# Kernel tuning notes

Hardware: AMD Instinct MI355X
Metric: run time of the kernel (lower is better)

The kernel has to match this reference:

```python
import jax, jax.numpy as jnp
import numpy as np

BN_EPS = 1e-5


def setup_inputs() -> dict:
    key = jax.random.key(0)
    ks = jax.random.split(key, 6)
    B, C, K, N = 4, 64, 16, 16384  # batch, feat channels, neighbors, points
    W_OUT = 16  # weightnet output channels (fixed by Linear(16*mlp[-1], ...))
    xyz = jax.random.normal(ks[0], (B, N, 3), dtype=jnp.float32)
    points = jax.random.normal(ks[1], (B, C, K, N), dtype=jnp.float32)
    coordinate = jax.random.normal(ks[2], (B, 3, K, N), dtype=jnp.float32)
    w1 = jax.random.normal(ks[3], (W_OUT, 3), dtype=jnp.float32) * 0.5
    b1 = jnp.zeros((W_OUT,), dtype=jnp.float32)
    lin_w = jax.random.normal(ks[4], (C, W_OUT * C), dtype=jnp.float32) * (1.0 / np.sqrt(W_OUT * C))
    lin_b = jnp.zeros((C,), dtype=jnp.float32)
    gamma = jnp.ones((C,), dtype=jnp.float32)
    beta = jnp.zeros((C,), dtype=jnp.float32)
    return {"xyz": xyz, "points": points, "coordinate": coordinate,
            "w1": w1, "b1": b1, "lin_w": lin_w, "lin_b": lin_b,
            "gamma": gamma, "beta": beta}


def reference(xyz, points, coordinate, w1, b1, lin_w, lin_b, gamma, beta):
    B, C, K, N = points.shape
    # weightnet: 1x1 conv (3 -> 16) + ReLU over coordinate [B,3,K,N] -> [B,16,K,N]
    weights = jax.nn.relu(jnp.einsum('oc,bckn->bokn', w1, coordinate) + b1[None, :, None, None])
    # per-point aggregation: [B,N,C,K] @ [B,N,K,16] -> [B,N,C,16]
    new_points = jnp.einsum('bckn,bokn->bnco', points, weights)
    new_points = new_points.reshape(B, N, C * 16)  # [B, N, 16*C]
    # linear projection 16*C -> C
    new_points = jnp.einsum('bnk,ok->bno', new_points, lin_w) + lin_b  # [B, N, C]
    # BatchNorm1d over channel dim (training-mode batch stats), layout [B, C, N]
    new_points = new_points.transpose(0, 2, 1)  # [B, C, N]
    mean = jnp.mean(new_points, axis=(0, 2), keepdims=True)
    var = jnp.var(new_points, axis=(0, 2), keepdims=True)
    new_points = (new_points - mean) * jax.lax.rsqrt(var + BN_EPS)
    new_points = new_points * gamma[None, :, None] + beta[None, :, None]
    new_points = jax.nn.relu(new_points)  # [B, C, N]
    return (xyz, new_points)
```

## Files before the change

kernel.cpp:

```cpp
#include <hip/hip_runtime.h>

#define BB 4
#define CC 64
#define KK 16
#define NN 16384
#define NT 64
#define CH 8
#define KS 128

typedef __attribute__((ext_vector_type(8))) short short8;
typedef __attribute__((ext_vector_type(4))) float floatx4;

__device__ __forceinline__ unsigned short f2bf(float x) {
    unsigned u = __builtin_bit_cast(unsigned, x);
    u += 0x7FFFu + ((u >> 16) & 1u);
    return (unsigned short)(u >> 16);
}
__device__ __forceinline__ float bflo(unsigned u) {
    return __builtin_bit_cast(float, u << 16);
}
__device__ __forceinline__ float bfhi(unsigned u) {
    return __builtin_bit_cast(float, u & 0xFFFF0000u);
}

__global__ __launch_bounds__(256, 2)
void fused_main(const float* __restrict__ points,
                const float* __restrict__ coordinate,
                const float* __restrict__ w1,
                const float* __restrict__ b1,
                const float* __restrict__ lin_w,
                float* __restrict__ y_out)
{
    __shared__ __align__(16) unsigned short s_p[CH][NT][24];
    __shared__ __align__(16) unsigned short s_a[NT][KS + 8];
    __shared__ __align__(16) unsigned short s_w[CC][KS + 8];

    const int t    = threadIdx.x;
    const int lane = t & 63;
    const int q    = __builtin_amdgcn_readfirstlane(t >> 6);
    const int r    = lane & 15;
    const int s    = lane >> 4;

    const int bid = blockIdx.x;
    const int b   = bid >> 8;
    const int n0  = (bid & 255) * NT;

    float wreg[4][KK];
    {
        const float* coordB = coordinate + (size_t)b * 3 * KK * NN + n0 + lane;
        float c0[KK], c1[KK], c2[KK];
        #pragma unroll
        for (int k = 0; k < KK; ++k) {
            c0[k] = coordB[(0 * KK + k) * NN];
            c1[k] = coordB[(1 * KK + k) * NN];
            c2[k] = coordB[(2 * KK + k) * NN];
        }
        #pragma unroll
        for (int j = 0; j < 4; ++j) {
            const int o = 4 * q + j;
            const float w1x = w1[o * 3 + 0];
            const float w1y = w1[o * 3 + 1];
            const float w1z = w1[o * 3 + 2];
            const float bo  = b1[o];
            #pragma unroll
            for (int k = 0; k < KK; ++k) {
                float v = fmaf(w1x, c0[k], fmaf(w1y, c1[k], fmaf(w1z, c2[k], bo)));
                wreg[j][k] = fmaxf(v, 0.0f);
            }
        }
    }

    floatx4 acc[4];
    #pragma unroll
    for (int nt = 0; nt < 4; ++nt) acc[nt] = (floatx4){0.f, 0.f, 0.f, 0.f};

    const float* pB = points + (size_t)b * CC * KK * NN + n0;

    for (int c8 = 0; c8 < CC; c8 += CH) {
        __syncthreads();

        #pragma unroll
        for (int w = 0; w < 8; ++w) {
            const int idx = w * 256 + t;
            const int c_l = idx >> 8;
            const int k   = (idx >> 4) & 15;
            const int n4  = (idx & 15) * 4;
            const float4 v =
                *(const float4*)(pB + ((size_t)(c8 + c_l) * KK + k) * NN + n4);
            s_p[c_l][n4 + 0][k] = f2bf(v.x);
            s_p[c_l][n4 + 1][k] = f2bf(v.y);
            s_p[c_l][n4 + 2][k] = f2bf(v.z);
            s_p[c_l][n4 + 3][k] = f2bf(v.w);
        }
        #pragma unroll
        for (int w = 0; w < 8; ++w) {
            const int idx = w * 256 + t;
            const int oc  = idx >> 5;
            const int k4  = (idx & 31) * 4;
            const float4 v =
                *(const float4*)(lin_w + (size_t)oc * 1024 + c8 * 16 + k4);
            ushort4 pk;
            pk.x = f2bf(v.x); pk.y = f2bf(v.y); pk.z = f2bf(v.z); pk.w = f2bf(v.w);
            *(ushort4*)&s_w[oc][k4] = pk;
        }
        __syncthreads();

        #pragma unroll
        for (int c_l = 0; c_l < CH; ++c_l) {
            const uint4 u0 = *(const uint4*)&s_p[c_l][lane][0];
            const uint4 u1 = *(const uint4*)&s_p[c_l][lane][8];
            float p16[16];
            p16[0]  = bflo(u0.x); p16[1]  = bfhi(u0.x);
            p16[2]  = bflo(u0.y); p16[3]  = bfhi(u0.y);
            p16[4]  = bflo(u0.z); p16[5]  = bfhi(u0.z);
            p16[6]  = bflo(u0.w); p16[7]  = bfhi(u0.w);
            p16[8]  = bflo(u1.x); p16[9]  = bfhi(u1.x);
            p16[10] = bflo(u1.y); p16[11] = bfhi(u1.y);
            p16[12] = bflo(u1.z); p16[13] = bfhi(u1.z);
            p16[14] = bflo(u1.w); p16[15] = bfhi(u1.w);
            float a4[4];
            #pragma unroll
            for (int j = 0; j < 4; ++j) {
                float a = 0.f;
                #pragma unroll
                for (int k = 0; k < KK; ++k) a = fmaf(p16[k], wreg[j][k], a);
                a4[j] = a;
            }
            ushort4 pk;
            pk.x = f2bf(a4[0]); pk.y = f2bf(a4[1]);
            pk.z = f2bf(a4[2]); pk.w = f2bf(a4[3]);
            *(ushort4*)&s_a[lane][c_l * 16 + 4 * q] = pk;
        }
        __syncthreads();

        #pragma unroll
        for (int kk = 0; kk < 4; ++kk) {
            const short8 af = *(const short8*)&s_a[16 * q + r][kk * 32 + s * 8];
            #pragma unroll
            for (int nt = 0; nt < 4; ++nt) {
                const short8 bf = *(const short8*)&s_w[nt * 16 + r][kk * 32 + s * 8];
                acc[nt] = __builtin_amdgcn_mfma_f32_16x16x32_bf16(af, bf, acc[nt], 0, 0, 0);
            }
        }
    }

    float* yB = y_out + (size_t)b * CC * NN + n0;
    #pragma unroll
    for (int nt = 0; nt < 4; ++nt) {
        const int oc = nt * 16 + r;
        const float4 v = make_float4(acc[nt][0], acc[nt][1], acc[nt][2], acc[nt][3]);
        *(float4*)(yB + (size_t)oc * NN + 16 * q + 4 * s) = v;
    }
}

__global__ __launch_bounds__(256)
void bn_reduce(const float* __restrict__ y, const float* __restrict__ gamma,
               const float* __restrict__ beta, float* __restrict__ ab)
{
    const int ch = blockIdx.x;
    const int t  = threadIdx.x;
    float s = 0.f, ss = 0.f;
    for (int b = 0; b < BB; ++b) {
        const float4* p = (const float4*)(y + ((size_t)b * CC + ch) * NN);
        for (int i = t; i < NN / 4; i += 256) {
            const float4 v = p[i];
            s  += v.x + v.y + v.z + v.w;
            ss += v.x * v.x + v.y * v.y + v.z * v.z + v.w * v.w;
        }
    }
    #pragma unroll
    for (int m = 1; m < 64; m <<= 1) {
        s  += __shfl_xor(s, m);
        ss += __shfl_xor(ss, m);
    }
    __shared__ float rs[4], rss[4];
    if ((t & 63) == 0) { rs[t >> 6] = s; rss[t >> 6] = ss; }
    __syncthreads();
    if (t == 0) {
        const float S  = rs[0] + rs[1] + rs[2] + rs[3];
        const float SS = rss[0] + rss[1] + rss[2] + rss[3];
        const float inv  = 1.0f / (float)(BB * NN);
        const float mean = S * inv;
        const float var  = SS * inv - mean * mean;
        const float a    = gamma[ch] * rsqrtf(var + 1e-5f);
        ab[ch]      = a;
        ab[CC + ch] = beta[ch] - mean * a;
    }
}

__global__ __launch_bounds__(256)
void bn_apply(float* __restrict__ y, const float* __restrict__ ab)
{
    const size_t i = (size_t)blockIdx.x * 256 + threadIdx.x;
    float4* p = (float4*)y;
    float4 v = p[i];
    const int ch = (int)((i * 4) >> 14) & 63;
    const float a = ab[ch], bb = ab[CC + ch];
    v.x = fmaxf(fmaf(a, v.x, bb), 0.0f);
    v.y = fmaxf(fmaf(a, v.y, bb), 0.0f);
    v.z = fmaxf(fmaf(a, v.z, bb), 0.0f);
    v.w = fmaxf(fmaf(a, v.w, bb), 0.0f);
    p[i] = v;
}

extern "C" void kernel_launch(void* const* d_in, const int* in_sizes, int n_in,
                              void* d_out, int out_size, void* d_ws, size_t ws_size,
                              hipStream_t stream)
{
    const float* xyz        = (const float*)d_in[0];
    const float* points     = (const float*)d_in[1];
    const float* coordinate = (const float*)d_in[2];
    const float* w1         = (const float*)d_in[3];
    const float* b1         = (const float*)d_in[4];
    const float* lin_w      = (const float*)d_in[5];
    const float* gamma      = (const float*)d_in[7];
    const float* beta       = (const float*)d_in[8];

    float* out = (float*)d_out;
    float* ws  = (float*)d_ws;

    const size_t xyz_elems = (size_t)BB * NN * 3;

    hipMemcpyAsync(out, xyz, xyz_elems * sizeof(float),
                   hipMemcpyDeviceToDevice, stream);

    float* y_out = out + xyz_elems;

    fused_main<<<BB * (NN / NT), 256, 0, stream>>>(
        points, coordinate, w1, b1, lin_w, y_out);
    bn_reduce<<<CC, 256, 0, stream>>>(y_out, gamma, beta, ws);
    bn_apply<<<(BB * CC * NN) / 4 / 256, 256, 0, stream>>>(y_out, ws);
}
```

Measured before the change: 488.5 us.

## Load points directly to registers, prepack lin_w fragments, split BN reduce

```diff
diff --git a/kernel.cpp b/kernel.cpp
--- a/kernel.cpp
+++ b/kernel.cpp
@@ -6,46 +6,77 @@
 #define NN 16384
 #define NT 64
 #define CH 8
-#define KS 128
+#define NCH 8
 
 typedef __attribute__((ext_vector_type(8))) short short8;
 typedef __attribute__((ext_vector_type(4))) float floatx4;
-
-__device__ __forceinline__ unsigned short f2bf(float x) {
+typedef __attribute__((ext_vector_type(2))) _Float16 half2v;
+
+__device__ __forceinline__ unsigned short f2bf_rtne(float x) {
     unsigned u = __builtin_bit_cast(unsigned, x);
     u += 0x7FFFu + ((u >> 16) & 1u);
     return (unsigned short)(u >> 16);
 }
-__device__ __forceinline__ float bflo(unsigned u) {
-    return __builtin_bit_cast(float, u << 16);
-}
-__device__ __forceinline__ float bfhi(unsigned u) {
-    return __builtin_bit_cast(float, u & 0xFFFF0000u);
-}
-
-__global__ __launch_bounds__(256, 2)
+
+__device__ __forceinline__ unsigned pack_bf16x2(float lo, float hi) {
+    unsigned a = __builtin_bit_cast(unsigned, lo) + 0x8000u;
+    unsigned b = __builtin_bit_cast(unsigned, hi) + 0x8000u;
+    return __builtin_amdgcn_perm(b, a, 0x07060302u);
+}
+
+__device__ __forceinline__ half2v cvt2h(float a, float b) {
+    return __builtin_bit_cast(half2v, __builtin_amdgcn_cvt_pkrtz(a, b));
+}
+
+#if __has_builtin(__builtin_amdgcn_fdot2)
+#define DOT2(a, b, c) __builtin_amdgcn_fdot2((a), (b), (c), false)
+#else
+__device__ __forceinline__ float dot2_fb(half2v a, half2v b, float c) {
+    return fmaf((float)a[0], (float)b[0], fmaf((float)a[1], (float)b[1], c));
+}
+#define DOT2(a, b, c) dot2_fb((a), (b), (c))
+#endif
+
+__global__ __launch_bounds__(256)
+void prep_bfrag(const float* __restrict__ lin_w, unsigned short* __restrict__ bfrag)
+{
+    const int tid  = blockIdx.x * 256 + threadIdx.x;
+    const int lane = tid & 63;
+    const int g    = tid >> 6;
+    const int ci   = g >> 4;
+    const int kk   = (g >> 2) & 3;
+    const int nt   = g & 3;
+    const int r    = lane & 15;
+    const int sq   = lane >> 4;
+
+    const float* src = lin_w + (size_t)(nt * 16 + r) * 1024 + ci * 128 + kk * 32 + sq * 8;
+    unsigned short v[8];
+    #pragma unroll
+    for (int j = 0; j < 8; ++j) v[j] = f2bf_rtne(src[j]);
+    *(uint4*)(bfrag + ((size_t)g * 64 + lane) * 8) = *(const uint4*)v;
+}
+
+__global__ __launch_bounds__(256, 4)
 void fused_main(const float* __restrict__ points,
                 const float* __restrict__ coordinate,
                 const float* __restrict__ w1,
                 const float* __restrict__ b1,
-                const float* __restrict__ lin_w,
+                const unsigned short* __restrict__ bfrag,
                 float* __restrict__ y_out)
 {
-    __shared__ __align__(16) unsigned short s_p[CH][NT][24];
-    __shared__ __align__(16) unsigned short s_a[NT][KS + 8];
-    __shared__ __align__(16) unsigned short s_w[CC][KS + 8];
+    __shared__ __align__(16) unsigned short s_a[NT][136];
 
     const int t    = threadIdx.x;
     const int lane = t & 63;
     const int q    = __builtin_amdgcn_readfirstlane(t >> 6);
     const int r    = lane & 15;
-    const int s    = lane >> 4;
+    const int sq   = lane >> 4;
 
     const int bid = blockIdx.x;
     const int b   = bid >> 8;
     const int n0  = (bid & 255) * NT;
 
-    float wreg[4][KK];
+    half2v wh[4][8];
     {
         const float* coordB = coordinate + (size_t)b * 3 * KK * NN + n0 + lane;
         float c0[KK], c1[KK], c2[KK];
@@ -63,9 +94,10 @@
             const float w1z = w1[o * 3 + 2];
             const float bo  = b1[o];
             #pragma unroll
-            for (int k = 0; k < KK; ++k) {
-                float v = fmaf(w1x, c0[k], fmaf(w1y, c1[k], fmaf(w1z, c2[k], bo)));
-                wreg[j][k] = fmaxf(v, 0.0f);
+            for (int kp = 0; kp < 8; ++kp) {
+                float v0 = fmaf(w1x, c0[2 * kp],     fmaf(w1y, c1[2 * kp],     fmaf(w1z, c2[2 * kp],     bo)));
+                float v1 = fmaf(w1x, c0[2 * kp + 1], fmaf(w1y, c1[2 * kp + 1], fmaf(w1z, c2[2 * kp + 1], bo)));
+                wh[j][kp] = cvt2h(fmaxf(v0, 0.0f), fmaxf(v1, 0.0f));
             }
         }
     }
@@ -74,71 +106,45 @@
     #pragma unroll
     for (int nt = 0; nt < 4; ++nt) acc[nt] = (floatx4){0.f, 0.f, 0.f, 0.f};
 
-    const float* pB = points + (size_t)b * CC * KK * NN + n0;
-
-    for (int c8 = 0; c8 < CC; c8 += CH) {
-        __syncthreads();
-
-        #pragma unroll
-        for (int w = 0; w < 8; ++w) {
-            const int idx = w * 256 + t;
-            const int c_l = idx >> 8;
-            const int k   = (idx >> 4) & 15;
-            const int n4  = (idx & 15) * 4;
-            const float4 v =
-                *(const float4*)(pB + ((size_t)(c8 + c_l) * KK + k) * NN + n4);
-            s_p[c_l][n4 + 0][k] = f2bf(v.x);
-            s_p[c_l][n4 + 1][k] = f2bf(v.y);
-            s_p[c_l][n4 + 2][k] = f2bf(v.z);
-            s_p[c_l][n4 + 3][k] = f2bf(v.w);
-        }
-        #pragma unroll
-        for (int w = 0; w < 8; ++w) {
-            const int idx = w * 256 + t;
-            const int oc  = idx >> 5;
-            const int k4  = (idx & 31) * 4;
-            const float4 v =
-                *(const float4*)(lin_w + (size_t)oc * 1024 + c8 * 16 + k4);
-            ushort4 pk;
-            pk.x = f2bf(v.x); pk.y = f2bf(v.y); pk.z = f2bf(v.z); pk.w = f2bf(v.w);
-            *(ushort4*)&s_w[oc][k4] = pk;
-        }
-        __syncthreads();
-
-        #pragma unroll
-        for (int c_l = 0; c_l < CH; ++c_l) {
-            const uint4 u0 = *(const uint4*)&s_p[c_l][lane][0];
-            const uint4 u1 = *(const uint4*)&s_p[c_l][lane][8];
-            float p16[16];
-            p16[0]  = bflo(u0.x); p16[1]  = bfhi(u0.x);
-            p16[2]  = bflo(u0.y); p16[3]  = bfhi(u0.y);
-            p16[4]  = bflo(u0.z); p16[5]  = bfhi(u0.z);
-            p16[6]  = bflo(u0.w); p16[7]  = bfhi(u0.w);
-            p16[8]  = bflo(u1.x); p16[9]  = bfhi(u1.x);
-            p16[10] = bflo(u1.y); p16[11] = bfhi(u1.y);
-            p16[12] = bflo(u1.z); p16[13] = bfhi(u1.z);
-            p16[14] = bflo(u1.w); p16[15] = bfhi(u1.w);
+    const float* pB = points + (size_t)b * CC * KK * NN + n0 + lane;
+
+    for (int ci = 0; ci < NCH; ++ci) {
+        uint2 packA[CH];
+        #pragma unroll
+        for (int cl = 0; cl < CH; ++cl) {
+            const float* pc = pB + (size_t)(ci * CH + cl) * KK * NN;
+            float pv[KK];
+            #pragma unroll
+            for (int k = 0; k < KK; ++k) pv[k] = pc[(size_t)k * NN];
+            half2v ph[8];
+            #pragma unroll
+            for (int kp = 0; kp < 8; ++kp)
+                ph[kp] = cvt2h(pv[2 * kp], pv[2 * kp + 1]);
             float a4[4];
             #pragma unroll
             for (int j = 0; j < 4; ++j) {
                 float a = 0.f;
                 #pragma unroll
-                for (int k = 0; k < KK; ++k) a = fmaf(p16[k], wreg[j][k], a);
+                for (int kp = 0; kp < 8; ++kp) a = DOT2(ph[kp], wh[j][kp], a);
                 a4[j] = a;
             }
-            ushort4 pk;
-            pk.x = f2bf(a4[0]); pk.y = f2bf(a4[1]);
-            pk.z = f2bf(a4[2]); pk.w = f2bf(a4[3]);
-            *(ushort4*)&s_a[lane][c_l * 16 + 4 * q] = pk;
-        }
+            packA[cl].x = pack_bf16x2(a4[0], a4[1]);
+            packA[cl].y = pack_bf16x2(a4[2], a4[3]);
+        }
+
         __syncthreads();
+        #pragma unroll
+        for (int cl = 0; cl < CH; ++cl)
+            *(uint2*)&s_a[lane][cl * 16 + 4 * q] = packA[cl];
+        __syncthreads();
 
         #pragma unroll
         for (int kk = 0; kk < 4; ++kk) {
-            const short8 af = *(const short8*)&s_a[16 * q + r][kk * 32 + s * 8];
+            const short8 af = *(const short8*)&s_a[16 * q + r][kk * 32 + sq * 8];
             #pragma unroll
             for (int nt = 0; nt < 4; ++nt) {
-                const short8 bf = *(const short8*)&s_w[nt * 16 + r][kk * 32 + s * 8];
+                const short8 bf = *(const short8*)
+                    (bfrag + ((((size_t)ci * 4 + kk) * 4 + nt) * 64 + lane) * 8);
                 acc[nt] = __builtin_amdgcn_mfma_f32_16x16x32_bf16(af, bf, acc[nt], 0, 0, 0);
             }
         }
@@ -149,24 +155,22 @@
     for (int nt = 0; nt < 4; ++nt) {
         const int oc = nt * 16 + r;
         const float4 v = make_float4(acc[nt][0], acc[nt][1], acc[nt][2], acc[nt][3]);
-        *(float4*)(yB + (size_t)oc * NN + 16 * q + 4 * s) = v;
+        *(float4*)(yB + (size_t)oc * NN + 16 * q + 4 * sq) = v;
     }
 }
 
 __global__ __launch_bounds__(256)
-void bn_reduce(const float* __restrict__ y, const float* __restrict__ gamma,
-               const float* __restrict__ beta, float* __restrict__ ab)
-{
-    const int ch = blockIdx.x;
+void bn_reduce(const float* __restrict__ y, float* __restrict__ part)
+{
+    const int ch = blockIdx.x & 63;
+    const int b  = blockIdx.x >> 6;
     const int t  = threadIdx.x;
+    const float4* p = (const float4*)(y + ((size_t)b * CC + ch) * NN);
     float s = 0.f, ss = 0.f;
-    for (int b = 0; b < BB; ++b) {
-        const float4* p = (const float4*)(y + ((size_t)b * CC + ch) * NN);
-        for (int i = t; i < NN / 4; i += 256) {
-            const float4 v = p[i];
-            s  += v.x + v.y + v.z + v.w;
-            ss += v.x * v.x + v.y * v.y + v.z * v.z + v.w * v.w;
-        }
+    for (int i = t; i < NN / 4; i += 256) {
+        const float4 v = p[i];
+        s  += v.x + v.y + v.z + v.w;
+        ss += v.x * v.x + v.y * v.y + v.z * v.z + v.w * v.w;
     }
     #pragma unroll
     for (int m = 1; m < 64; m <<= 1) {
@@ -177,15 +181,29 @@
     if ((t & 63) == 0) { rs[t >> 6] = s; rss[t >> 6] = ss; }
     __syncthreads();
     if (t == 0) {
-        const float S  = rs[0] + rs[1] + rs[2] + rs[3];
-        const float SS = rss[0] + rss[1] + rss[2] + rss[3];
-        const float inv  = 1.0f / (float)(BB * NN);
-        const float mean = S * inv;
-        const float var  = SS * inv - mean * mean;
-        const float a    = gamma[ch] * rsqrtf(var + 1e-5f);
-        ab[ch]      = a;
-        ab[CC + ch] = beta[ch] - mean * a;
-    }
+        part[blockIdx.x]       = rs[0] + rs[1] + rs[2] + rs[3];
+        part[256 + blockIdx.x] = rss[0] + rss[1] + rss[2] + rss[3];
+    }
+}
+
+__global__ void bn_stats(const float* __restrict__ part,
+                         const float* __restrict__ gamma,
+                         const float* __restrict__ beta,
+                         float* __restrict__ ab)
+{
+    const int ch = threadIdx.x;
+    float S = 0.f, SS = 0.f;
+    #pragma unroll
+    for (int b = 0; b < BB; ++b) {
+        S  += part[b * 64 + ch];
+        SS += part[256 + b * 64 + ch];
+    }
+    const float inv  = 1.0f / (float)(BB * NN);
+    const float mean = S * inv;
+    const float var  = SS * inv - mean * mean;
+    const float a    = gamma[ch] * rsqrtf(var + 1e-5f);
+    ab[ch]      = a;
+    ab[CC + ch] = beta[ch] - mean * a;
 }
 
 __global__ __launch_bounds__(256)
@@ -217,17 +235,21 @@
     const float* beta       = (const float*)d_in[8];
 
     float* out = (float*)d_out;
-    float* ws  = (float*)d_ws;
+
+    unsigned short* bfrag = (unsigned short*)d_ws;
+    float* part = (float*)d_ws + 32768;
+    float* ab   = part + 512;
 
     const size_t xyz_elems = (size_t)BB * NN * 3;
-
-    hipMemcpyAsync(out, xyz, xyz_elems * sizeof(float),
-                   hipMemcpyDeviceToDevice, stream);
+    (void)hipMemcpyAsync(out, xyz, xyz_elems * sizeof(float),
+                         hipMemcpyDeviceToDevice, stream);
 
     float* y_out = out + xyz_elems;
 
+    prep_bfrag<<<32, 256, 0, stream>>>(lin_w, bfrag);
     fused_main<<<BB * (NN / NT), 256, 0, stream>>>(
-        points, coordinate, w1, b1, lin_w, y_out);
-    bn_reduce<<<CC, 256, 0, stream>>>(y_out, gamma, beta, ws);
-    bn_apply<<<(BB * CC * NN) / 4 / 256, 256, 0, stream>>>(y_out, ws);
-}
+        points, coordinate, w1, b1, bfrag, y_out);
+    bn_reduce<<<BB * CC, 256, 0, stream>>>(y_out, part);
+    bn_stats<<<1, 64, 0, stream>>>(part, gamma, beta, ab);
+    bn_apply<<<(BB * CC * NN) / 4 / 256, 256, 0, stream>>>(y_out, ab);
+}
```

After: 458.7 us. 1.07x faster.
